# Optimization experiments

Measured on AMD Instinct MI355X. Metric: run time of the kernel, lower is better.

Reference implementation:

```python
import jax, jax.numpy as jnp
import numpy as np

C_IN = 64
H = 32          # h_channels
HEADS = 8
HC = H * HEADS  # 256
C_OUT = 64
EPS = 1e-5


def conv1x1(w, x):
    # 1x1 Conv1d == per-position GEMM: w [O, C], x [B, C, L] -> [B, O, L]
    return jnp.einsum('oc,bcl->bol', w, x)


def batchnorm1d(x, gamma, beta):
    # training-mode BatchNorm1d: stats over (batch, length), biased variance
    mean = jnp.mean(x, axis=(0, 2), keepdims=True)
    var = jnp.mean(jnp.square(x - mean), axis=(0, 2), keepdims=True)
    xhat = (x - mean) * jax.lax.rsqrt(var + EPS)
    return xhat * gamma[None, :, None] + beta[None, :, None]


def setup_inputs() -> dict:
    key = jax.random.key(0)
    ks = jax.random.split(key, 6)
    B, L = 16, 8192
    s_in = 1.0 / np.sqrt(C_IN)
    s_hc = 1.0 / np.sqrt(HC)
    return {
        'x':  jax.random.normal(ks[0], (B, C_IN, L), dtype=jnp.float32),
        'wk': jax.random.uniform(ks[1], (HC, C_IN), jnp.float32, -s_in, s_in),
        'wq': jax.random.uniform(ks[2], (HC, C_IN), jnp.float32, -s_in, s_in),
        'wv': jax.random.uniform(ks[3], (HC, C_IN), jnp.float32, -s_in, s_in),
        'wc': jax.random.uniform(ks[4], (C_IN, HC), jnp.float32, -s_hc, s_hc),
        'g1': jnp.ones((C_IN,), jnp.float32),
        'b1': jnp.zeros((C_IN,), jnp.float32),
        'wl': jax.random.uniform(ks[5], (C_OUT, C_IN), jnp.float32, -s_in, s_in),
        'g2': jnp.ones((C_OUT,), jnp.float32),
        'b2': jnp.zeros((C_OUT,), jnp.float32),
    }


def reference(x, wk, wq, wv, wc, g1, b1, wl, g2, b2):
    k = conv1x1(wk, x)  # [B, HC, L]
    q = conv1x1(wq, x)
    v = conv1x1(wv, x)
    # channel-wise attention: q @ k^T over length -> [B, HC, HC]
    scores = jnp.einsum('bil,bjl->bij', q, k)
    attn = jax.nn.softmax(scores, axis=1)  # softmax over dim=1 (rows), as in source
    att_vec = jnp.einsum('bij,bjl->bil', attn, v) / np.sqrt(H).astype(np.float32)
    out = conv1x1(wc, att_vec)            # [B, C_IN, L]
    out = batchnorm1d(out, g1, b1) + x    # residual
    out = batchnorm1d(conv1x1(wl, out), g2, b2)
    return jax.nn.relu(out)
```

## Files before the change

### kernel.cpp

```cpp
#include <hip/hip_runtime.h>
#include <math.h>

#define TB 16
#define TL 8192
#define TC 64

constexpr float INV_BL = 1.0f / (16.0f * 8192.0f);
constexpr float EPSV = 1e-5f;
constexpr float INV_SQRT_H = 0.17677669529663687f;

#define WS_G      0
#define WS_SX     65536
#define WS_STATS  66560
#define WS_M      66816
#define WS_N      132352
#define WS_S1T    197888
#define WS_V1P    460032
#define WS_GPART  4654336
#define WS_SXPART 8848640
#define WS_MPART  8914176

typedef __attribute__((ext_vector_type(8))) short short8v;
typedef __attribute__((ext_vector_type(4))) float f32x4;

__device__ __forceinline__ ushort bf16rne(float f){
  uint u = __float_as_uint(f);
  u += 0x7FFF + ((u >> 16) & 1);
  return (ushort)(u >> 16);
}

__device__ __forceinline__ int fraddr(int ch, int g){
  return ch*128 + 8*(g ^ (ch & 7));
}

__global__ __launch_bounds__(256) void k1_gram(const float* __restrict__ x,
                                               float* __restrict__ ws){
  __shared__ ushort Xh[64*128];
  __shared__ ushort Xl[64*128];
  const int b = blockIdx.y, chunk = blockIdx.x;
  const int t = threadIdx.x;
  const int lane = t & 63;
  const int w = __builtin_amdgcn_readfirstlane(t >> 6);
  const float* xb = x + (size_t)b*TC*TL + (size_t)chunk*128;
  const int ch = t >> 2, q = t & 3;
  float sx = 0.f;
  #pragma unroll
  for (int gg=0; gg<4; ++gg){
    const float4 v0 = *(const float4*)(xb + ch*TL + q*32 + 8*gg);
    const float4 v1 = *(const float4*)(xb + ch*TL + q*32 + 8*gg + 4);
    const float ff[8] = {v0.x,v0.y,v0.z,v0.w,v1.x,v1.y,v1.z,v1.w};
    union { short8v v; ushort u[8]; } hh, ll;
    #pragma unroll
    for (int i=0;i<8;++i){
      sx += ff[i];
      const ushort hv = bf16rne(ff[i]);
      hh.u[i] = hv;
      ll.u[i] = bf16rne(ff[i] - __uint_as_float(((uint)hv)<<16));
    }
    const int g = q*4 + gg;
    const int wa = ch*128 + 8*(g ^ (ch & 7));
    *(short8v*)&Xh[wa] = hh.v;
    *(short8v*)&Xl[wa] = ll.v;
  }
  __syncthreads();
  const int rA = w*16 + (lane & 15);
  const int gq = lane >> 4;
  f32x4 acc0={0.f,0.f,0.f,0.f}, acc1={0.f,0.f,0.f,0.f},
        acc2={0.f,0.f,0.f,0.f}, acc3={0.f,0.f,0.f,0.f};
  #pragma unroll
  for (int kk=0; kk<4; ++kk){
    const int g = kk*4 + gq;
    const short8v Ah = *(const short8v*)&Xh[fraddr(rA, g)];
    const short8v Al = *(const short8v*)&Xl[fraddr(rA, g)];
    const int rB = (lane & 15);
    const short8v Bh0 = *(const short8v*)&Xh[fraddr(rB,      g)];
    const short8v Bl0 = *(const short8v*)&Xl[fraddr(rB,      g)];
    const short8v Bh1 = *(const short8v*)&Xh[fraddr(rB + 16, g)];
    const short8v Bl1 = *(const short8v*)&Xl[fraddr(rB + 16, g)];
    const short8v Bh2 = *(const short8v*)&Xh[fraddr(rB + 32, g)];
    const short8v Bl2 = *(const short8v*)&Xl[fraddr(rB + 32, g)];
    const short8v Bh3 = *(const short8v*)&Xh[fraddr(rB + 48, g)];
    const short8v Bl3 = *(const short8v*)&Xl[fraddr(rB + 48, g)];
    acc0 = __builtin_amdgcn_mfma_f32_16x16x32_bf16(Ah, Bh0, acc0, 0, 0, 0);
    acc0 = __builtin_amdgcn_mfma_f32_16x16x32_bf16(Ah, Bl0, acc0, 0, 0, 0);
    acc0 = __builtin_amdgcn_mfma_f32_16x16x32_bf16(Al, Bh0, acc0, 0, 0, 0);
    acc0 = __builtin_amdgcn_mfma_f32_16x16x32_bf16(Al, Bl0, acc0, 0, 0, 0);
    acc1 = __builtin_amdgcn_mfma_f32_16x16x32_bf16(Ah, Bh1, acc1, 0, 0, 0);
    acc1 = __builtin_amdgcn_mfma_f32_16x16x32_bf16(Ah, Bl1, acc1, 0, 0, 0);
    acc1 = __builtin_amdgcn_mfma_f32_16x16x32_bf16(Al, Bh1, acc1, 0, 0, 0);
    acc1 = __builtin_amdgcn_mfma_f32_16x16x32_bf16(Al, Bl1, acc1, 0, 0, 0);
    acc2 = __builtin_amdgcn_mfma_f32_16x16x32_bf16(Ah, Bh2, acc2, 0, 0, 0);
    acc2 = __builtin_amdgcn_mfma_f32_16x16x32_bf16(Ah, Bl2, acc2, 0, 0, 0);
    acc2 = __builtin_amdgcn_mfma_f32_16x16x32_bf16(Al, Bh2, acc2, 0, 0, 0);
    acc2 = __builtin_amdgcn_mfma_f32_16x16x32_bf16(Al, Bl2, acc2, 0, 0, 0);
    acc3 = __builtin_amdgcn_mfma_f32_16x16x32_bf16(Ah, Bh3, acc3, 0, 0, 0);
    acc3 = __builtin_amdgcn_mfma_f32_16x16x32_bf16(Ah, Bl3, acc3, 0, 0, 0);
    acc3 = __builtin_amdgcn_mfma_f32_16x16x32_bf16(Al, Bh3, acc3, 0, 0, 0);
    acc3 = __builtin_amdgcn_mfma_f32_16x16x32_bf16(Al, Bl3, acc3, 0, 0, 0);
  }
  float* Gp = ws + WS_GPART + (size_t)(b*64 + chunk)*4096;
  const int col = lane & 15, rq = lane >> 4;
  #pragma unroll
  for (int r=0;r<4;++r){
    const int row = (w*16 + rq*4 + r)*64;
    Gp[row +  0 + col] = acc0[r];
    Gp[row + 16 + col] = acc1[r];
    Gp[row + 32 + col] = acc2[r];
    Gp[row + 48 + col] = acc3[r];
  }
  sx += __shfl_xor(sx, 1, 4);
  sx += __shfl_xor(sx, 2, 4);
  if (q == 0){
    ws[WS_SXPART + (b*64+chunk)*64 + ch] = sx;
  }
}

__global__ __launch_bounds__(256) void kA1(float* __restrict__ ws){
  const int p = blockIdx.x, b = blockIdx.y;
  const int t = threadIdx.x;
  const float* Gp = ws + WS_GPART + (size_t)b*64*4096 + p*256 + t;
  float s = 0.f;
  #pragma unroll 8
  for (int ch=0; ch<64; ++ch) s += Gp[(size_t)ch*4096];
  ws[WS_G + b*4096 + p*256 + t] = s;
  if (p==0 && t<64){
    float sv = 0.f;
    #pragma unroll 8
    for (int ch=0; ch<64; ++ch) sv += ws[WS_SXPART + (b*64+ch)*64 + t];
    ws[WS_SX + b*64 + t] = sv;
  }
  if (p==0 && b==0) ws[WS_STATS + t] = 0.f;
}

__global__ __launch_bounds__(256) void kA2(const float* __restrict__ wq,
                                           float* __restrict__ ws){
  __shared__ float Gt[64*68];
  const int b = blockIdx.y, iblk = blockIdx.x;
  const int t = threadIdx.x;
  const float* G = ws + WS_G + b*4096;
  #pragma unroll
  for (int r=0;r<4;++r){
    const int idx = r*1024 + t*4;
    *(float4*)&Gt[(idx>>6)*68 + (idx&63)] = *(const float4*)(G + idx);
  }
  __syncthreads();
  const int il = t>>2, cq = t&3;
  const int i = iblk*64 + il;
  const float* wqr = wq + i*64;
  float4 a0={0,0,0,0}, a1={0,0,0,0}, a2={0,0,0,0}, a3={0,0,0,0};
  #pragma unroll 8
  for (int k=0;k<64;++k){
    const float a = wqr[k];
    const float4 g0 = *(const float4*)&Gt[k*68 + cq*16 + 0];
    const float4 g1 = *(const float4*)&Gt[k*68 + cq*16 + 4];
    const float4 g2 = *(const float4*)&Gt[k*68 + cq*16 + 8];
    const float4 g3 = *(const float4*)&Gt[k*68 + cq*16 + 12];
    a0.x=fmaf(a,g0.x,a0.x); a0.y=fmaf(a,g0.y,a0.y); a0.z=fmaf(a,g0.z,a0.z); a0.w=fmaf(a,g0.w,a0.w);
    a1.x=fmaf(a,g1.x,a1.x); a1.y=fmaf(a,g1.y,a1.y); a1.z=fmaf(a,g1.z,a1.z); a1.w=fmaf(a,g1.w,a1.w);
    a2.x=fmaf(a,g2.x,a2.x); a2.y=fmaf(a,g2.y,a2.y); a2.z=fmaf(a,g2.z,a2.z); a2.w=fmaf(a,g2.w,a2.w);
    a3.x=fmaf(a,g3.x,a3.x); a3.y=fmaf(a,g3.y,a3.y); a3.z=fmaf(a,g3.z,a3.z); a3.w=fmaf(a,g3.w,a3.w);
  }
  float* S1T = ws + WS_S1T + b*16384;
  const int c0 = cq*16;
  S1T[(c0+ 0)*256 + i]=a0.x; S1T[(c0+ 1)*256 + i]=a0.y; S1T[(c0+ 2)*256 + i]=a0.z; S1T[(c0+ 3)*256 + i]=a0.w;
  S1T[(c0+ 4)*256 + i]=a1.x; S1T[(c0+ 5)*256 + i]=a1.y; S1T[(c0+ 6)*256 + i]=a1.z; S1T[(c0+ 7)*256 + i]=a1.w;
  S1T[(c0+ 8)*256 + i]=a2.x; S1T[(c0+ 9)*256 + i]=a2.y; S1T[(c0+10)*256 + i]=a2.z; S1T[(c0+11)*256 + i]=a2.w;
  S1T[(c0+12)*256 + i]=a3.x; S1T[(c0+13)*256 + i]=a3.y; S1T[(c0+14)*256 + i]=a3.z; S1T[(c0+15)*256 + i]=a3.w;
}

__global__ __launch_bounds__(256) void kb12(const float* __restrict__ wk,
                                            const float* __restrict__ wv,
                                            float* __restrict__ ws){
  __shared__ float scl[256*17];
  __shared__ float pstat[256];
  __shared__ float fstat[32];
  const int b = blockIdx.y, jp = blockIdx.x;
  const int j0 = jp*16;
  const int t = threadIdx.x;
  const float* S1Tb = ws + WS_S1T + b*16384;
  float sc[16];
  #pragma unroll
  for (int jj=0;jj<16;++jj) sc[jj]=0.f;
  #pragma unroll 2
  for (int k=0;k<64;++k){
    const float s1 = S1Tb[k*256 + t];
    const float* wkr = wk + j0*64 + k;
    #pragma unroll
    for (int jj=0;jj<16;++jj)
      sc[jj] = fmaf(wkr[jj*64], s1, sc[jj]);
  }
  #pragma unroll
  for (int jj=0;jj<16;++jj) scl[t*17+jj] = sc[jj];
  __syncthreads();
  const int col = t&15, ig = t>>4;
  {
    float m = -3.0e38f;
    #pragma unroll
    for (int q=0;q<16;++q) m = fmaxf(m, scl[(ig*16+q)*17 + col]);
    pstat[ig*16+col] = m;
  }
  __syncthreads();
  if (t<16){
    float m = -3.0e38f;
    #pragma unroll
    for (int q=0;q<16;++q) m = fmaxf(m, pstat[q*16+t]);
    fstat[t] = m;
  }
  __syncthreads();
  {
    const float mj = fstat[col];
    float s = 0.f;
    #pragma unroll
    for (int q=0;q<16;++q) s += __expf(scl[(ig*16+q)*17 + col] - mj);
    pstat[ig*16+col] = s;
  }
  __syncthreads();
  if (t<16){
    float s = 0.f;
    #pragma unroll
    for (int q=0;q<16;++q) s += pstat[q*16+t];
    fstat[16+t] = 1.f/s;
  }
  __syncthreads();
  #pragma unroll
  for (int jj=0;jj<16;++jj)
    sc[jj] = __expf(sc[jj] - fstat[jj]) * fstat[16+jj];
  float* Vp = ws + WS_V1P + (size_t)(b*16 + jp)*16384;
  for (int cb=0; cb<4; ++cb){
    float acc[16];
    #pragma unroll
    for (int cc=0;cc<16;++cc) acc[cc]=0.f;
    #pragma unroll
    for (int jj=0;jj<16;++jj){
      const float p = sc[jj];
      const float* wvr = wv + (j0+jj)*64 + cb*16;
      #pragma unroll
      for (int cc=0;cc<16;++cc)
        acc[cc] = fmaf(p, wvr[cc], acc[cc]);
    }
    #pragma unroll
    for (int cc=0;cc<16;++cc)
      Vp[(cb*16+cc)*256 + t] = acc[cc];
  }
}

__global__ __launch_bounds__(256) void kc_mpart(const float* __restrict__ wc,
                                                float* __restrict__ ws){
  __shared__ float V1l[16*65];
  const int b = blockIdx.y, kq = blockIdx.x;
  const int t = threadIdx.x;
  #pragma unroll
  for (int r=0;r<4;++r){
    const int e = t + 256*r;
    const int il = e & 15, c = e >> 4;
    const float* Vp = ws + WS_V1P + (size_t)b*16*16384 + c*256 + kq*16 + il;
    float s = 0.f;
    #pragma unroll
    for (int jp=0;jp<16;++jp) s += Vp[jp*16384];
    V1l[il*65 + c] = s * INV_SQRT_H;
  }
  __syncthreads();
  const int c = t & 63;
  const int og = __builtin_amdgcn_readfirstlane(t >> 6);
  float acc[16];
  #pragma unroll
  for (int oo=0;oo<16;++oo) acc[oo]=0.f;
  #pragma unroll
  for (int il=0; il<16; ++il){
    const float v = V1l[il*65 + c];
    const float* wcr = wc + (og*16)*256 + kq*16 + il;
    #pragma unroll
    for (int oo=0;oo<16;++oo)
      acc[oo] = fmaf(wcr[oo*256], v, acc[oo]);
  }
  float* Mp = ws + WS_MPART + (size_t)(b*16 + kq)*4096;
  #pragma unroll
  for (int oo=0;oo<16;++oo)
    Mp[(og*16+oo)*64 + c] = acc[oo];
}

__global__ __launch_bounds__(256) void kd_stats1(float* __restrict__ ws){
  __shared__ float Msub[4*65];
  __shared__ float Gl[64*67];
  __shared__ float Sxl[64];
  const int b = blockIdx.y, oq = blockIdx.x;
  const int t = threadIdx.x;
  const int o = t >> 6, lane = t & 63;
  const int row = oq*4 + o;
  {
    const float* Mp = ws + WS_MPART + (size_t)b*16*4096 + row*64 + lane;
    float s = 0.f;
    #pragma unroll
    for (int kq=0;kq<16;++kq) s += Mp[kq*4096];
    ws[WS_M + b*4096 + row*64 + lane] = s;
    Msub[o*65 + lane] = s;
  }
  #pragma unroll
  for (int r=0;r<16;++r){
    const int e = t + 256*r;
    Gl[(e>>6)*67 + (e&63)] = ws[WS_G + b*4096 + e];
  }
  if (t<64) Sxl[t] = ws[WS_SX + b*64 + t];
  __syncthreads();
  float sk = 0.f;
  #pragma unroll 4
  for (int c=0;c<64;++c) sk = fmaf(Gl[lane*67+c], Msub[o*65+c], sk);
  float d = Msub[o*65 + lane] * sk;
  float s1 = Msub[o*65 + lane] * Sxl[lane];
  #pragma unroll
  for (int off=1; off<64; off<<=1){
    d  += __shfl_xor(d,  off);
    s1 += __shfl_xor(s1, off);
  }
  if (lane==0){
    atomicAdd(&ws[WS_STATS + row], s1);
    atomicAdd(&ws[WS_STATS + 64 + row], d);
  }
}

__global__ __launch_bounds__(256) void ke_n_stats2(const float* __restrict__ wl,
                                                   const float* __restrict__ g1,
                                                   float* __restrict__ ws){
  __shared__ float Ml[64*65];
  __shared__ float Gl[64*67];
  __shared__ float Nsub[4*65];
  __shared__ float Sxl[64], a1l[64];
  const int b = blockIdx.y, oq = blockIdx.x;
  const int t = threadIdx.x;
  const int o = t >> 6, lane = t & 63;
  const int row = oq*4 + o;
  if (t<64){
    const float mean1 = ws[WS_STATS+t]*INV_BL;
    const float var1 = ws[WS_STATS+64+t]*INV_BL - mean1*mean1;
    a1l[t] = g1[t]*rsqrtf(var1 + EPSV);
    Sxl[t] = ws[WS_SX + b*64 + t];
  }
  #pragma unroll
  for (int r=0;r<16;++r){
    const int e = t + 256*r;
    Ml[(e>>6)*65 + (e&63)] = ws[WS_M + b*4096 + e];
    Gl[(e>>6)*67 + (e&63)] = ws[WS_G + b*4096 + e];
  }
  __syncthreads();
  float acc = 0.f;
  #pragma unroll 4
  for (int k=0;k<64;++k){
    const float wk_ = wl[row*64 + k] * a1l[k];
    acc = fmaf(wk_, Ml[k*65 + lane], acc);
  }
  const float nv = acc + wl[row*64 + lane];
  ws[WS_N + b*4096 + row*64 + lane] = nv;
  Nsub[o*65 + lane] = nv;
  __syncthreads();
  float sk = 0.f;
  #pragma unroll 4
  for (int c=0;c<64;++c) sk = fmaf(Gl[lane*67+c], Nsub[o*65+c], sk);
  float d = Nsub[o*65 + lane] * sk;
  float s2 = Nsub[o*65 + lane] * Sxl[lane];
  #pragma unroll
  for (int off=1; off<64; off<<=1){
    d  += __shfl_xor(d,  off);
    s2 += __shfl_xor(s2, off);
  }
  if (lane==0){
    atomicAdd(&ws[WS_STATS + 128 + row], s2);
    atomicAdd(&ws[WS_STATS + 192 + row], d);
  }
}

__global__ __launch_bounds__(512) void k3_out(const float* __restrict__ x,
                                              const float* __restrict__ g2,
                                              const float* __restrict__ b2,
                                              const float* __restrict__ ws,
                                              float* __restrict__ out){
  __shared__ float a2l[64], el[64];
  const int b = blockIdx.y, lc = blockIdx.x;
  const int t = threadIdx.x;
  if (t<64){
    const float mu = ws[WS_STATS+128+t]*INV_BL;
    const float var2 = ws[WS_STATS+192+t]*INV_BL - mu*mu;
    const float a2 = g2[t]*rsqrtf(var2 + EPSV);
    a2l[t] = a2;
    el[t] = b2[t] - a2*mu;
  }
  __syncthreads();
  const int w = __builtin_amdgcn_readfirstlane(t >> 6);
  const int lane = t & 63;
  const int l = lc*256 + 4*lane;
  const float* Np = ws + WS_N + b*4096 + w*8*64;
  const float* xb = x + (size_t)b*TC*TL + l;
  float4 acc[8];
  #pragma unroll
  for (int oo=0;oo<8;++oo){ acc[oo].x=0.f; acc[oo].y=0.f; acc[oo].z=0.f; acc[oo].w=0.f; }
  #pragma unroll 8
  for (int c=0;c<64;++c){
    const float4 xv = *(const float4*)(xb + (size_t)c*TL);
    #pragma unroll
    for (int oo=0;oo<8;++oo){
      const float nv = Np[oo*64 + c];
      acc[oo].x = fmaf(nv, xv.x, acc[oo].x);
      acc[oo].y = fmaf(nv, xv.y, acc[oo].y);
      acc[oo].z = fmaf(nv, xv.z, acc[oo].z);
      acc[oo].w = fmaf(nv, xv.w, acc[oo].w);
    }
  }
  #pragma unroll
  for (int oo=0;oo<8;++oo){
    const float a2v = a2l[w*8+oo], ev = el[w*8+oo];
    float4 r;
    r.x = fmaxf(fmaf(a2v, acc[oo].x, ev), 0.f);
    r.y = fmaxf(fmaf(a2v, acc[oo].y, ev), 0.f);
    r.z = fmaxf(fmaf(a2v, acc[oo].z, ev), 0.f);
    r.w = fmaxf(fmaf(a2v, acc[oo].w, ev), 0.f);
    *(float4*)(out + (size_t)(b*TC + w*8 + oo)*TL + l) = r;
  }
}

extern "C" void kernel_launch(void* const* d_in, const int* in_sizes, int n_in,
                              void* d_out, int out_size, void* d_ws, size_t ws_size,
                              hipStream_t stream){
  const float* x  = (const float*)d_in[0];
  const float* wk = (const float*)d_in[1];
  const float* wq = (const float*)d_in[2];
  const float* wv = (const float*)d_in[3];
  const float* wc = (const float*)d_in[4];
  const float* g1 = (const float*)d_in[5];
  const float* wl = (const float*)d_in[7];
  const float* g2 = (const float*)d_in[8];
  const float* b2 = (const float*)d_in[9];
  float* out = (float*)d_out;
  float* ws  = (float*)d_ws;

  k1_gram    <<<dim3(64,16), 256, 0, stream>>>(x, ws);
  kA1        <<<dim3(16,16), 256, 0, stream>>>(ws);
  kA2        <<<dim3(4,16),  256, 0, stream>>>(wq, ws);
  kb12       <<<dim3(16,16), 256, 0, stream>>>(wk, wv, ws);
  kc_mpart   <<<dim3(16,16), 256, 0, stream>>>(wc, ws);
  kd_stats1  <<<dim3(16,16), 256, 0, stream>>>(ws);
  ke_n_stats2<<<dim3(16,16), 256, 0, stream>>>(wl, g1, ws);
  k3_out     <<<dim3(32,16), 512, 0, stream>>>(x, g2, b2, ws, out);
}
```

Measured before the change: 101.1 us.

## Move final output GEMM onto bf16 MFMA with split-precision hi/lo emulation

The final kernel, which applies the fused per-batch weight matrix to x and then the BN2+ReLU epilogue, now runs on MFMA bf16 instructions instead of scalar FP32 FMAs. Both the weights and x are split into bf16 high and low parts and combined with four MFMAs, which keeps accuracy close to fp32. x tiles are transposed through LDS and the grid is retiled to 128-length blocks of 256 threads. The cost is extra LDS traffic and conversion work, plus scalar (non-vectorized) output stores that may hurt write coalescing in a kernel that is mostly memory-bound.

Result: no change. 99.65 us (-1.4%).

```diff
diff --git a/kernel.cpp b/kernel.cpp
--- a/kernel.cpp
+++ b/kernel.cpp
@@ -368,11 +368,14 @@
   }
 }
 
-__global__ __launch_bounds__(512) void k3_out(const float* __restrict__ x,
+__global__ __launch_bounds__(256) void k3_out(const float* __restrict__ x,
                                               const float* __restrict__ g2,
                                               const float* __restrict__ b2,
                                               const float* __restrict__ ws,
                                               float* __restrict__ out){
+  __shared__ float xlT[128*68];
+  __shared__ ushort Nh[64*72];
+  __shared__ ushort Nl[64*72];
   __shared__ float a2l[64], el[64];
   const int b = blockIdx.y, lc = blockIdx.x;
   const int t = threadIdx.x;
@@ -383,36 +386,87 @@
     a2l[t] = a2;
     el[t] = b2[t] - a2*mu;
   }
+  {
+    const float* Nsrc = ws + WS_N + b*4096;
+    #pragma unroll
+    for (int r=0;r<16;++r){
+      const int e = t + 256*r;
+      const int o = e>>6, c = e&63;
+      const float nv = Nsrc[e];
+      const ushort h = bf16rne(nv);
+      Nh[o*72 + c] = h;
+      Nl[o*72 + c] = bf16rne(nv - __uint_as_float(((uint)h)<<16));
+    }
+  }
+  {
+    const float* xw = x + (size_t)b*TC*TL + lc*128;
+    const int ch = t>>2, q = t&3;
+    #pragma unroll
+    for (int i=0;i<8;++i){
+      const int l0 = q*32 + i*4;
+      const float4 v = *(const float4*)(xw + (size_t)ch*TL + l0);
+      xlT[(l0+0)*68 + ch] = v.x;
+      xlT[(l0+1)*68 + ch] = v.y;
+      xlT[(l0+2)*68 + ch] = v.z;
+      xlT[(l0+3)*68 + ch] = v.w;
+    }
+  }
   __syncthreads();
   const int w = __builtin_amdgcn_readfirstlane(t >> 6);
   const int lane = t & 63;
-  const int l = lc*256 + 4*lane;
-  const float* Np = ws + WS_N + b*4096 + w*8*64;
-  const float* xb = x + (size_t)b*TC*TL + l;
-  float4 acc[8];
-  #pragma unroll
-  for (int oo=0;oo<8;++oo){ acc[oo].x=0.f; acc[oo].y=0.f; acc[oo].z=0.f; acc[oo].w=0.f; }
-  #pragma unroll 8
-  for (int c=0;c<64;++c){
-    const float4 xv = *(const float4*)(xb + (size_t)c*TL);
-    #pragma unroll
-    for (int oo=0;oo<8;++oo){
-      const float nv = Np[oo*64 + c];
-      acc[oo].x = fmaf(nv, xv.x, acc[oo].x);
-      acc[oo].y = fmaf(nv, xv.y, acc[oo].y);
-      acc[oo].z = fmaf(nv, xv.z, acc[oo].z);
-      acc[oo].w = fmaf(nv, xv.w, acc[oo].w);
-    }
-  }
-  #pragma unroll
-  for (int oo=0;oo<8;++oo){
-    const float a2v = a2l[w*8+oo], ev = el[w*8+oo];
-    float4 r;
-    r.x = fmaxf(fmaf(a2v, acc[oo].x, ev), 0.f);
-    r.y = fmaxf(fmaf(a2v, acc[oo].y, ev), 0.f);
-    r.z = fmaxf(fmaf(a2v, acc[oo].z, ev), 0.f);
-    r.w = fmaxf(fmaf(a2v, acc[oo].w, ev), 0.f);
-    *(float4*)(out + (size_t)(b*TC + w*8 + oo)*TL + l) = r;
+  const int orow = lane & 15, gq = lane >> 4;
+  short8v NhF[8], NlF[8];
+  #pragma unroll
+  for (int ot=0; ot<4; ++ot){
+    #pragma unroll
+    for (int ks=0; ks<2; ++ks){
+      const int o = ot*16 + orow;
+      const int cb = ks*32 + gq*8;
+      NhF[ot*2+ks] = *(const short8v*)&Nh[o*72 + cb];
+      NlF[ot*2+ks] = *(const short8v*)&Nl[o*72 + cb];
+    }
+  }
+  f32x4 acc[8];
+  #pragma unroll
+  for (int i=0;i<8;++i){ acc[i][0]=0.f; acc[i][1]=0.f; acc[i][2]=0.f; acc[i][3]=0.f; }
+  #pragma unroll
+  for (int lt=0; lt<2; ++lt){
+    const int lrow = (w*2+lt)*16 + orow;
+    #pragma unroll
+    for (int ks=0; ks<2; ++ks){
+      const int cb = ks*32 + gq*8;
+      float xv[8];
+      *(float4*)&xv[0] = *(const float4*)&xlT[lrow*68 + cb];
+      *(float4*)&xv[4] = *(const float4*)&xlT[lrow*68 + cb + 4];
+      union { short8v v; ushort u[8]; } bh, bl;
+      #pragma unroll
+      for (int j=0;j<8;++j){
+        const ushort h = bf16rne(xv[j]);
+        bh.u[j] = h;
+        bl.u[j] = bf16rne(xv[j] - __uint_as_float(((uint)h)<<16));
+      }
+      #pragma unroll
+      for (int ot=0; ot<4; ++ot){
+        acc[lt*4+ot] = __builtin_amdgcn_mfma_f32_16x16x32_bf16(NhF[ot*2+ks], bh.v, acc[lt*4+ot], 0, 0, 0);
+        acc[lt*4+ot] = __builtin_amdgcn_mfma_f32_16x16x32_bf16(NhF[ot*2+ks], bl.v, acc[lt*4+ot], 0, 0, 0);
+        acc[lt*4+ot] = __builtin_amdgcn_mfma_f32_16x16x32_bf16(NlF[ot*2+ks], bh.v, acc[lt*4+ot], 0, 0, 0);
+        acc[lt*4+ot] = __builtin_amdgcn_mfma_f32_16x16x32_bf16(NlF[ot*2+ks], bl.v, acc[lt*4+ot], 0, 0, 0);
+      }
+    }
+  }
+  const int lbase = lc*128;
+  #pragma unroll
+  for (int lt=0; lt<2; ++lt){
+    const int l = lbase + (w*2+lt)*16 + orow;
+    #pragma unroll
+    for (int ot=0; ot<4; ++ot){
+      #pragma unroll
+      for (int r=0;r<4;++r){
+        const int o = ot*16 + gq*4 + r;
+        const float v = fmaxf(fmaf(a2l[o], acc[lt*4+ot][r], el[o]), 0.f);
+        out[(size_t)(b*TC + o)*TL + l] = v;
+      }
+    }
   }
 }
 
@@ -438,5 +492,5 @@
   kc_mpart   <<<dim3(16,16), 256, 0, stream>>>(wc, ws);
   kd_stats1  <<<dim3(16,16), 256, 0, stream>>>(ws);
   ke_n_stats2<<<dim3(16,16), 256, 0, stream>>>(wl, g1, ws);
-  k3_out     <<<dim3(32,16), 512, 0, stream>>>(x, g2, b2, ws, out);
-}
+  k3_out     <<<dim3(64,16), 256, 0, stream>>>(x, g2, b2, ws, out);
+}
```
